# Performance work log

Hardware: AMD Instinct MI355X
Metric: run time of the kernel (lower is better)

The kernel has to match this reference:

```python
import jax, jax.numpy as jnp
import numpy as np
import math

POOLED_H = 2
POOLED_W = 64  # fixed: rois constructed so maxratio = POOLED_W / POOLED_H
NH = 256
NCLASS = 12  # len('0123456789.') + 1
C_IN = 512


def make_lstm_params(key, n_in, n_hidden):
    # torch nn.LSTM bidirectional: per direction W_ih [4H, in], W_hh [4H, H], b_ih, b_hh
    ks = jax.random.split(key, 8)
    s_i = 1.0 / np.sqrt(n_hidden)
    def u(k, shape):
        return jax.random.uniform(k, shape, jnp.float32, -s_i, s_i)
    p = {}
    for d, off in (('fw', 0), ('bw', 4)):
        p[d] = {
            'W_ih': u(ks[off + 0], (4 * n_hidden, n_in)),
            'W_hh': u(ks[off + 1], (4 * n_hidden, n_hidden)),
            'b_ih': u(ks[off + 2], (4 * n_hidden,)),
            'b_hh': u(ks[off + 3], (4 * n_hidden,)),
        }
    return p


def lstm_scan(x, p, n_hidden, reverse=False):
    # x: [T, B, n_in] -> [T, B, n_hidden]
    T, B, _ = x.shape
    W_ih, W_hh = p['W_ih'], p['W_hh']
    b = p['b_ih'] + p['b_hh']
    xg = jnp.einsum('tbi,gi->tbg', x, W_ih) + b  # [T,B,4H]

    def step(carry, xg_t):
        h, c = carry
        gates = xg_t + h @ W_hh.T
        i, f, g, o = jnp.split(gates, 4, axis=-1)
        i = jax.nn.sigmoid(i); f = jax.nn.sigmoid(f)
        g = jnp.tanh(g); o = jax.nn.sigmoid(o)
        c = f * c + i * g
        h = o * jnp.tanh(c)
        return (h, c), h

    h0 = jnp.zeros((B, n_hidden), x.dtype)
    c0 = jnp.zeros((B, n_hidden), x.dtype)
    _, hs = jax.lax.scan(step, (h0, c0), xg, reverse=reverse)
    return hs


def bilstm(x, p, n_hidden, W_emb, b_emb):
    hf = lstm_scan(x, p['fw'], n_hidden, reverse=False)
    hb = lstm_scan(x, p['bw'], n_hidden, reverse=True)
    h = jnp.concatenate([hf, hb], axis=-1)  # [T,B,2H]
    return h @ W_emb.T + b_emb


def roi_pool(base_feat, rois, pooled_h, pooled_w):
    # rois: [N,5] = [batch_idx, x1, y1, x2, y2] in feature coords (already scaled)
    # torch RoIPool: max pool over adaptive bins (spatial_scale=1).
    B, C, H, W = base_feat.shape

    def pool_one(roi):
        bi = roi[0].astype(jnp.int32)
        x1 = jnp.round(roi[1]).astype(jnp.int32)
        y1 = jnp.round(roi[2]).astype(jnp.int32)
        x2 = jnp.round(roi[3]).astype(jnp.int32)
        y2 = jnp.round(roi[4]).astype(jnp.int32)
        rw = jnp.maximum(x2 - x1 + 1, 1).astype(jnp.float32)
        rh = jnp.maximum(y2 - y1 + 1, 1).astype(jnp.float32)
        bin_h = rh / pooled_h
        bin_w = rw / pooled_w
        feat = base_feat[bi]  # [C,H,W]

        ph = jnp.arange(pooled_h)
        pw = jnp.arange(pooled_w)
        hstart = jnp.clip(jnp.floor(ph * bin_h).astype(jnp.int32) + y1, 0, H)
        hend = jnp.clip(jnp.ceil((ph + 1) * bin_h).astype(jnp.int32) + y1, 0, H)
        wstart = jnp.clip(jnp.floor(pw * bin_w).astype(jnp.int32) + x1, 0, W)
        wend = jnp.clip(jnp.ceil((pw + 1) * bin_w).astype(jnp.int32) + x1, 0, W)

        hh = jnp.arange(H)[None, :]
        ww = jnp.arange(W)[None, :]
        hmask = (hh >= hstart[:, None]) & (hh < hend[:, None])  # [ph,H]
        wmask = (ww >= wstart[:, None]) & (ww < wend[:, None])  # [pw,W]
        mask = hmask[:, None, :, None] & wmask[None, :, None, :]  # [ph,pw,H,W]
        neg = jnp.float32(-1e30)
        masked = jnp.where(mask[None], feat[:, None, None, :, :], neg)  # [C,ph,pw,H,W]
        pooled = masked.max(axis=(-2, -1))
        empty = ~mask.any(axis=(-2, -1))  # [ph,pw]
        return jnp.where(empty[None], 0.0, pooled)  # [C,ph,pw]

    return jax.vmap(pool_one)(rois)  # [N,C,ph,pw]


def setup_inputs() -> dict:
    key = jax.random.key(0)
    ks = jax.random.split(key, 10)
    B, C, H, W = 8, C_IN, 40, 160
    N = 32
    base_feat = jax.random.normal(ks[0], (B, C, H, W), jnp.float32)

    # rois normalized [bidx, x1, y1, x2, y2]; build so max aspect ratio = 32 -> pooled_w=64
    bidx = jax.random.randint(ks[1], (N,), 0, B).astype(jnp.float32)
    x1 = jax.random.uniform(ks[2], (N,), jnp.float32, 0.0, 0.3)
    y1 = jax.random.uniform(ks[3], (N,), jnp.float32, 0.0, 0.5)
    hgt = jax.random.uniform(ks[4], (N,), jnp.float32, 0.1, 0.3)
    # width/height ratio in normalized coords; after scaling by (W=160,H=40) feature
    # dims, ratio in feat coords = (w_n*160)/(h_n*40) = 4*w_n/h_n. Force max = 32.
    ratio = jax.random.uniform(ks[5], (N,), jnp.float32, 4.0, 32.0)
    ratio = ratio.at[0].set(32.0)
    wid_feat = ratio * (hgt * H)  # width in feature pixels
    wid = jnp.minimum(wid_feat / W, 0.99 - x1)
    # recompute so ratio exactly 32 at max: clamp keeps maxratio <= 32; pin roi 0
    wid = wid.at[0].set(jnp.minimum(32.0 * hgt[0] * H / W, 0.99 - x1[0]))
    hgt = hgt.at[0].set(wid[0] * W / (32.0 * H))
    x2 = x1 + wid
    y2 = jnp.minimum(y1 + hgt, 0.99)
    rois = jnp.stack([bidx, x1, y1, x2, y2], axis=1)

    text_length = jax.random.randint(ks[6], (1, N), 1, 8)
    text = jax.random.randint(ks[7], (1, 256), 1, NCLASS)  # labels 1..11

    # params
    p1 = make_lstm_params(ks[8], 1024, NH)
    p2 = make_lstm_params(ks[9], NH, NH)
    ke = jax.random.split(jax.random.key(1), 4)
    s1 = 1.0 / np.sqrt(2 * NH)
    W_emb1 = jax.random.uniform(ke[0], (NH, 2 * NH), jnp.float32, -s1, s1)
    b_emb1 = jax.random.uniform(ke[1], (NH,), jnp.float32, -s1, s1)
    W_emb2 = jax.random.uniform(ke[2], (NCLASS, 2 * NH), jnp.float32, -s1, s1)
    b_emb2 = jax.random.uniform(ke[3], (NCLASS,), jnp.float32, -s1, s1)

    params = {}
    for li, p in ((1, p1), (2, p2)):
        for d in ('fw', 'bw'):
            for n in ('W_ih', 'W_hh', 'b_ih', 'b_hh'):
                params[f'l{li}_{d}_{n}'] = p[d][n]
    params['W_emb1'] = W_emb1; params['b_emb1'] = b_emb1
    params['W_emb2'] = W_emb2; params['b_emb2'] = b_emb2

    return dict(base_feat=base_feat, text=text, text_length=text_length, rois=rois, **params)


def ctc_loss_sum(log_probs, labels, label_lengths):
    # log_probs: [T, B, K] log-softmax; labels: [B, Lmax] padded; blank = 0
    # standard CTC forward algorithm; returns sum of -log p over batch
    T, B, K = log_probs.shape
    Lmax = labels.shape[1]
    S = 2 * Lmax + 1
    # extended label sequence: blank, l1, blank, l2, ..., blank
    ext = jnp.zeros((B, S), jnp.int32)
    ext = ext.at[:, 1::2].set(labels.astype(jnp.int32))
    pos = jnp.arange(S)
    valid = pos[None, :] < (2 * label_lengths[:, None] + 1)

    # transition allowances
    same_as_2back = jnp.concatenate(
        [jnp.zeros((B, 2), bool), ext[:, 2:] == ext[:, :-2]], axis=1)
    is_blank = (ext == 0)
    allow_skip = (~is_blank) & (~same_as_2back)

    neg_inf = jnp.float32(-1e30)
    emit = jnp.take_along_axis(
        log_probs.transpose(1, 0, 2), ext[:, None, :].repeat(T, 1), axis=2
    ).transpose(1, 0, 2)  # [T, B, S]

    alpha0 = jnp.full((B, S), neg_inf)
    alpha0 = alpha0.at[:, 0].set(emit[0, :, 0])
    alpha0 = alpha0.at[:, 1].set(jnp.where(label_lengths > 0, emit[0, :, 1], neg_inf))

    def step(alpha, emit_t):
        a_prev1 = jnp.concatenate([jnp.full((B, 1), neg_inf), alpha[:, :-1]], axis=1)
        a_prev2 = jnp.concatenate([jnp.full((B, 2), neg_inf), alpha[:, :-2]], axis=1)
        a_prev2 = jnp.where(allow_skip, a_prev2, neg_inf)
        m = jnp.maximum(alpha, jnp.maximum(a_prev1, a_prev2))
        s = (jnp.exp(alpha - m) + jnp.exp(a_prev1 - m) + jnp.exp(a_prev2 - m))
        new = m + jnp.log(s) + emit_t
        new = jnp.where(valid, new, neg_inf)
        return new, None

    alpha_T, _ = jax.lax.scan(step, alpha0, emit[1:])
    end1 = 2 * label_lengths  # last blank
    end2 = 2 * label_lengths - 1  # last label
    aT1 = jnp.take_along_axis(alpha_T, end1[:, None], axis=1)[:, 0]
    aT2 = jnp.take_along_axis(alpha_T, jnp.maximum(end2, 0)[:, None], axis=1)[:, 0]
    aT2 = jnp.where(label_lengths > 0, aT2, neg_inf)
    m = jnp.maximum(aT1, aT2)
    logp = m + jnp.log(jnp.exp(aT1 - m) + jnp.exp(aT2 - m))
    return -jnp.sum(logp)


def reference(base_feat, text, text_length, rois,
              l1_fw_W_ih, l1_fw_W_hh, l1_fw_b_ih, l1_fw_b_hh,
              l1_bw_W_ih, l1_bw_W_hh, l1_bw_b_ih, l1_bw_b_hh,
              l2_fw_W_ih, l2_fw_W_hh, l2_fw_b_ih, l2_fw_b_hh,
              l2_bw_W_ih, l2_bw_W_hh, l2_bw_b_ih, l2_bw_b_hh,
              W_emb1, b_emb1, W_emb2, b_emb2):
    B, C, H, W = base_feat.shape
    rois = rois.at[:, jnp.array([1, 3])].multiply(W)
    rois = rois.at[:, jnp.array([2, 4])].multiply(H)
    pooled = roi_pool(base_feat, rois, POOLED_H, POOLED_W)  # [N,C,2,pw]
    N = pooled.shape[0]
    rnn_in = pooled.reshape(N, C * POOLED_H, POOLED_W).transpose(2, 0, 1)  # [T,N,1024]

    p1 = {'fw': dict(W_ih=l1_fw_W_ih, W_hh=l1_fw_W_hh, b_ih=l1_fw_b_ih, b_hh=l1_fw_b_hh),
          'bw': dict(W_ih=l1_bw_W_ih, W_hh=l1_bw_W_hh, b_ih=l1_bw_b_ih, b_hh=l1_bw_b_hh)}
    p2 = {'fw': dict(W_ih=l2_fw_W_ih, W_hh=l2_fw_W_hh, b_ih=l2_fw_b_ih, b_hh=l2_fw_b_hh),
          'bw': dict(W_ih=l2_bw_W_ih, W_hh=l2_bw_W_hh, b_ih=l2_bw_b_ih, b_hh=l2_bw_b_hh)}
    h1 = bilstm(rnn_in, p1, NH, W_emb1, b_emb1)
    preds = bilstm(h1, p2, NH, W_emb2, b_emb2)  # [T,N,nclass]

    log_probs = jax.nn.log_softmax(preds, axis=-1)
    tl = text_length[0].astype(jnp.int32)  # [N]
    # unflatten labels: text[0] holds concatenated labels; build padded [N, Lmax]
    Lmax = 8
    offsets = jnp.concatenate([jnp.zeros((1,), jnp.int32), jnp.cumsum(tl)[:-1]])
    idx = offsets[:, None] + jnp.arange(Lmax)[None, :]
    idx = jnp.clip(idx, 0, text.shape[1] - 1)
    labels = jnp.where(jnp.arange(Lmax)[None, :] < tl[:, None],
                       text[0][idx].astype(jnp.int32), 0)
    loss = ctc_loss_sum(log_probs, labels, tl) / N
    return loss
```

## Files before the change

### kernel.cpp

```cpp
#include <hip/hip_runtime.h>
#include <math.h>

#define TSTEPS 64
#define NSEQ   32
#define FH     40
#define FW     160

#define OFF_XGB    0u
#define OFF_RNNB   2097152u
#define OFF_W12B   3145728u
#define OFF_W22B   4194304u
#define OFF_WE1B   4456448u
#define OFF_WE2B   4521984u
#define OFF_PB1    4525056u
#define OFF_PB2    4527104u
#define OFF_W8L1F  4529152u
#define OFF_W8L1B  4594688u
#define OFF_W8L2F  4660224u
#define OFF_W8L2B  4725760u
#define OFF_HCB1   4791296u
#define OFF_HCB2   5315584u
#define OFF_H1B    5839872u
#define OFF_PREDS  6102016u

typedef __attribute__((ext_vector_type(8))) short short8;
typedef __attribute__((ext_vector_type(4))) float f32x4;
typedef __attribute__((ext_vector_type(4))) unsigned short ushort4v;
typedef __attribute__((ext_vector_type(4))) unsigned uint4v;

static __device__ inline unsigned short bf16c(float x) {
  union { float f; unsigned u; } v; v.f = x;
  unsigned r = v.u + 0x7fff + ((v.u >> 16) & 1);
  return (unsigned short)(r >> 16);
}
static __device__ inline float b2f(unsigned short u) {
  union { unsigned u; float f; } v; v.u = ((unsigned)u) << 16;
  return v.f;
}
static __device__ inline unsigned pk_bf16(float lo, float hi) {
  unsigned r;
  asm("v_cvt_pk_bf16_f32 %0, %1, %2" : "=v"(r) : "v"(lo), "v"(hi));
  return r;
}
static __device__ inline unsigned char fp8c(float x) {
  union { float f; unsigned u; } v; v.f = x;
  unsigned s = (v.u >> 24) & 0x80;
  float ax = fabsf(x);
  if (ax < 0.015625f) return (unsigned char)s;
  if (ax >= 448.0f) return (unsigned char)(s | 0x7e);
  unsigned e = (v.u >> 23) & 0xff;
  unsigned m = v.u & 0x7fffff;
  unsigned r = m + 0x7ffff + ((m >> 20) & 1);
  if (r >> 23) { e += 1; r = 0; }
  unsigned m3 = (r >> 20) & 7;
  int ee = (int)e - 127 + 7;
  if (ee > 15) return (unsigned char)(s | 0x7e);
  return (unsigned char)(s | (ee << 3) | m3);
}
static __device__ inline unsigned pk4_fp8(float a, float b, float c, float d) {
#if __has_builtin(__builtin_amdgcn_cvt_pk_fp8_f32)
  int r = __builtin_amdgcn_cvt_pk_fp8_f32(a, b, 0, false);
  r = __builtin_amdgcn_cvt_pk_fp8_f32(c, d, r, true);
  return (unsigned)r;
#else
  return (unsigned)fp8c(a) | ((unsigned)fp8c(b) << 8)
       | ((unsigned)fp8c(c) << 16) | ((unsigned)fp8c(d) << 24);
#endif
}

__global__ __launch_bounds__(256) void prep_kernel(
    const float* __restrict__ w1f, const float* __restrict__ w1b,
    const float* __restrict__ w2f, const float* __restrict__ w2b,
    const float* __restrict__ we1, const float* __restrict__ we2,
    const float* __restrict__ wh1f, const float* __restrict__ wh1b,
    const float* __restrict__ wh2f, const float* __restrict__ wh2b,
    const float* __restrict__ b1fi, const float* __restrict__ b1fh,
    const float* __restrict__ b1bi, const float* __restrict__ b1bh,
    const float* __restrict__ b2fi, const float* __restrict__ b2fh,
    const float* __restrict__ b2bi, const float* __restrict__ b2bh,
    unsigned short* __restrict__ w12b, unsigned short* __restrict__ w22b,
    unsigned short* __restrict__ we1o, unsigned short* __restrict__ we2o,
    unsigned char* __restrict__ o8l1f, unsigned char* __restrict__ o8l1b,
    unsigned char* __restrict__ o8l2f, unsigned char* __restrict__ o8l2b,
    float* __restrict__ pb1, float* __restrict__ pb2) {
  int b = blockIdx.x, tid = threadIdx.x;
  if (b < 2048) {
    const float* src = (b < 1024) ? w1f : w1b;
    unsigned short* dst = w12b + (size_t)((b < 1024) ? 0 : 1048576);
    int i = (b & 1023) * 256 + tid;
    int row = i >> 8, c4 = i & 255;
    int orow = (row & 255) * 4 + (row >> 8);
    float4 v = ((const float4*)src)[i];
    ushort4v o; o[0]=bf16c(v.x); o[1]=bf16c(v.y); o[2]=bf16c(v.z); o[3]=bf16c(v.w);
    *(ushort4v*)(dst + (size_t)orow * 1024 + c4 * 4) = o;
  } else if (b < 2560) {
    int bb = b - 2048;
    const float* src = (bb < 256) ? w2f : w2b;
    unsigned short* dst = w22b + (size_t)((bb < 256) ? 0 : 262144);
    int i = (bb & 255) * 256 + tid;
    int row = i >> 6, c4 = i & 63;
    int orow = (row & 255) * 4 + (row >> 8);
    float4 v = ((const float4*)src)[i];
    ushort4v o; o[0]=bf16c(v.x); o[1]=bf16c(v.y); o[2]=bf16c(v.z); o[3]=bf16c(v.w);
    *(ushort4v*)(dst + (size_t)orow * 256 + c4 * 4) = o;
  } else if (b < 2688) {
    int i = (b - 2560) * 256 + tid;
    int j = i >> 7, c4 = (i & 127) * 4;
    ushort4v o;
#pragma unroll
    for (int q = 0; q < 4; ++q) {
      int c = c4 + q;
      int d = c >> 8, k = c & 255;
      int u = (k >> 6) + (k & 63) * 4;
      o[q] = bf16c(we1[(size_t)j * 512 + d * 256 + u]);
    }
    ((ushort4v*)we1o)[i] = o;
  } else if (b < 2694) {
    int i = (b - 2688) * 256 + tid;
    int j = i >> 7, c4 = (i & 127) * 4;
    ushort4v o;
#pragma unroll
    for (int q = 0; q < 4; ++q) {
      int c = c4 + q;
      int d = c >> 8, k = c & 255;
      int u = (k >> 6) + (k & 63) * 4;
      o[q] = bf16c(we2[(size_t)j * 512 + d * 256 + u]);
    }
    ((ushort4v*)we2o)[i] = o;
  } else if (b < 3718) {
    int bb = b - 2694;
    int which = bb >> 8;
    const float* src = (which == 0) ? wh1f : (which == 1) ? wh1b
                     : (which == 2) ? wh2f : wh2b;
    unsigned char* dst = (which == 0) ? o8l1f : (which == 1) ? o8l1b
                       : (which == 2) ? o8l2f : o8l2b;
    int idx = (bb & 255) * 256 + tid;
    int row = idx >> 6, k4 = (idx & 63) * 4;
    const float* r = src + (size_t)row * 256;
    unsigned o = 0;
#pragma unroll
    for (int j = 0; j < 4; ++j) {
      int kp = k4 + j;
      int u = (kp >> 6) + (kp & 63) * 4;
      o |= ((unsigned)fp8c(r[u] * 64.0f)) << (8 * j);
    }
    ((unsigned*)dst)[idx] = o;
  } else if (b < 3726) {
    int m = (b - 3718) * 256 + tid;
    int dirq = m >> 10, mloc = m & 1023;
    int r = (mloc & 3) * 256 + (mloc >> 2);
    pb1[m] = dirq ? (b1bi[r] + b1bh[r]) : (b1fi[r] + b1fh[r]);
  } else {
    int m = (b - 3726) * 256 + tid;
    int dirq = m >> 10, mloc = m & 1023;
    int r = (mloc & 3) * 256 + (mloc >> 2);
    pb2[m] = dirq ? (b2bi[r] + b2bh[r]) : (b2fi[r] + b2fh[r]);
  }
}

__global__ __launch_bounds__(256) void roi_pool_kernel(
    const float* __restrict__ feat, const float* __restrict__ rois,
    unsigned short* __restrict__ rnn) {
  int n  = blockIdx.x;
  int cg = blockIdx.y;
  int tid = threadIdx.x;
  int pw = tid & 63, ph = (tid >> 6) & 1, cl = tid >> 7;
  int c = cg * 2 + cl;

  const float* r = rois + n * 5;
  int bi = (int)r[0];
  int x1 = (int)rintf(r[1] * (float)FW);
  int y1 = (int)rintf(r[2] * (float)FH);
  int x2 = (int)rintf(r[3] * (float)FW);
  int y2 = (int)rintf(r[4] * (float)FH);
  float rw = fmaxf((float)(x2 - x1 + 1), 1.0f);
  float rh = fmaxf((float)(y2 - y1 + 1), 1.0f);
  float bin_h = rh * 0.5f;
  float bin_w = rw * (1.0f / 64.0f);

  int hs = min(max((int)floorf((float)ph * bin_h) + y1, 0), FH);
  int he = min(max((int)ceilf((float)(ph + 1) * bin_h) + y1, 0), FH);
  int wst = min(max((int)floorf((float)pw * bin_w) + x1, 0), FW);
  int wen = min(max((int)ceilf((float)(pw + 1) * bin_w) + x1, 0), FW);

  float m = -1e30f;
  bool nonempty = (hs < he) && (wst < wen);
  const float* f = feat + ((size_t)bi * 512 + c) * (FH * FW);
  for (int h = hs; h < he; ++h) {
    const float* fr = f + h * FW;
    for (int w = wst; w < wen; ++w) m = fmaxf(m, fr[w]);
  }
  float out = nonempty ? m : 0.0f;
  rnn[((size_t)pw * NSEQ + n) * 1024 + c * 2 + ph] = bf16c(out);
}

#define GPITCH 40
__global__ __launch_bounds__(256) void gemm_bf16(
    const unsigned short* __restrict__ A, const unsigned short* __restrict__ B,
    float* __restrict__ Cf, unsigned short* __restrict__ Cb,
    int M, int N, int K,
    const float* __restrict__ bm1, const float* __restrict__ bn, int mode) {
  __shared__ unsigned short Al[128 * GPITCH];
  __shared__ unsigned short Bl[128 * GPITCH];
  int m0 = blockIdx.y * 128, n0 = blockIdx.x * 128;
  int tid = threadIdx.x;
  int wid = tid >> 6, l = tid & 63, ln15 = l & 15, kg = l >> 4;
  int wm = wid >> 1, wn = wid & 1;

  f32x4 acc[4][4];
#pragma unroll
  for (int i = 0; i < 4; ++i)
#pragma unroll
    for (int j = 0; j < 4; ++j)
#pragma unroll
      for (int q = 0; q < 4; ++q) acc[i][j][q] = 0.0f;

  for (int k0 = 0; k0 < K; k0 += 32) {
#pragma unroll
    for (int it = 0; it < 2; ++it) {
      int chunk = tid + it * 256;
      int row = chunk >> 2, part = chunk & 3;
      short8 va = *(const short8*)(A + (size_t)(m0 + row) * K + k0 + part * 8);
      *(short8*)(Al + row * GPITCH + part * 8) = va;
      short8 vb;
      if (n0 + row < N) {
        vb = *(const short8*)(B + (size_t)(n0 + row) * K + k0 + part * 8);
      } else {
#pragma unroll
        for (int q = 0; q < 8; ++q) vb[q] = 0;
      }
      *(short8*)(Bl + row * GPITCH + part * 8) = vb;
    }
    __syncthreads();

    short8 a[4], b[4];
#pragma unroll
    for (int mt = 0; mt < 4; ++mt)
      a[mt] = *(const short8*)(Al + (wm * 64 + mt * 16 + ln15) * GPITCH + kg * 8);
#pragma unroll
    for (int nt = 0; nt < 4; ++nt)
      b[nt] = *(const short8*)(Bl + (wn * 64 + nt * 16 + ln15) * GPITCH + kg * 8);
#pragma unroll
    for (int mt = 0; mt < 4; ++mt)
#pragma unroll
      for (int nt = 0; nt < 4; ++nt)
        acc[mt][nt] = __builtin_amdgcn_mfma_f32_16x16x32_bf16(a[mt], b[nt], acc[mt][nt], 0, 0, 0);
    __syncthreads();
  }

  if (mode == 5) {
#pragma unroll
    for (int mt = 0; mt < 4; ++mt) {
      int mbase = m0 + wm * 64 + mt * 16 + kg * 4;
      f32x4 pbv = *(const f32x4*)(bm1 + mbase);
      int dirq = mbase >> 10;
      int unit = (mbase & 1023) >> 2;
#pragma unroll
      for (int nt = 0; nt < 4; ++nt) {
        int col = n0 + wn * 64 + nt * 16 + ln15;
        int t = col >> 5, n = col & 31;
        ushort4v q;
#pragma unroll
        for (int j = 0; j < 4; ++j)
          q[j] = bf16c((acc[mt][nt][j] + pbv[j]) * 1024.0f);
        *(ushort4v*)(Cb + (size_t)dirq * 2097152u + ((t << 8) + unit) * 128 + n * 4) = q;
      }
    }
    return;
  }

#pragma unroll
  for (int mt = 0; mt < 4; ++mt) {
#pragma unroll
    for (int j = 0; j < 4; ++j) {
      int m = m0 + wm * 64 + mt * 16 + kg * 4 + j;
      float bmv = bm1 ? bm1[m] : 0.0f;
#pragma unroll
      for (int nt = 0; nt < 4; ++nt) {
        int n = n0 + wn * 64 + nt * 16 + ln15;
        if (n < N) {
          float v = acc[mt][nt][j] + bmv;
          if (bn) v += bn[n];
          if (mode == 1) Cb[(size_t)m * N + n] = bf16c(v);
          else Cf[(size_t)m * N + n] = v;
        }
      }
    }
  }
}

__global__ __launch_bounds__(512, 2) void lstm_layer8(
    const unsigned short* __restrict__ xgb,
    const unsigned char* __restrict__ w8fw,
    const unsigned char* __restrict__ w8bw,
    unsigned short* __restrict__ hcatb) {
  const int dir = blockIdx.x >> 1;
  const int nbase = (blockIdx.x & 1) * 16;
  const int tid = threadIdx.x;
  const int w = tid >> 6;
  const int l = tid & 63;
  const int ln15 = l & 15;
  const int kg = l >> 4;
  const int u_wave = w * 32;

  __shared__ unsigned char h8[2][16][256];

  const unsigned char* W8 = dir ? w8bw : w8fw;

  unsigned long long afrag[8][8];
  {
    int gate = ln15 & 3, du = ln15 >> 2;
#pragma unroll
    for (int mt = 0; mt < 8; ++mt) {
      const unsigned char* wr = W8 + (size_t)((gate << 8) + u_wave + mt * 4 + du) * 256;
#pragma unroll
      for (int kc = 0; kc < 8; ++kc)
        afrag[mt][kc] = *(const unsigned long long*)(wr + kc * 32 + kg * 8);
    }
  }

  const unsigned short* xgd = xgb + (size_t)dir * 2097152u;
  const int lane_off = (nbase + ln15) * 4;
  float cst[8] = {0.f, 0.f, 0.f, 0.f, 0.f, 0.f, 0.f, 0.f};
  f32x4 acc[8];
  ushort4v xnext[8];

  {
    int t0 = dir ? 63 : 0;
    const unsigned short* xb = xgd + (size_t)t0 * 32768 + lane_off;
#pragma unroll
    for (int mt = 0; mt < 8; ++mt)
      xnext[mt] = *(const ushort4v*)(xb + (u_wave + mt * 4 + kg) * 128);
#pragma unroll
    for (int mt = 0; mt < 8; ++mt)
#pragma unroll
      for (int j = 0; j < 4; ++j) acc[mt][j] = b2f(xnext[mt][j]);
  }

  const int swzw = (ln15 & 7) << 4;
  const int myslot = kg * 64 + w * 8;
  const float kNI = -1.0f / 1024.0f;
  const float kP2 = 2.0f / 1024.0f;

  for (int s = 0; s < TSTEPS; ++s) {
    const int t = dir ? (63 - s) : s;
    const int p = s & 1;

    if (s < TSTEPS - 1) {
      int tn2 = dir ? (t - 1) : (t + 1);
      const unsigned short* xb = xgd + (size_t)tn2 * 32768 + lane_off;
#pragma unroll
      for (int mt = 0; mt < 8; ++mt)
        xnext[mt] = *(const ushort4v*)(xb + (u_wave + mt * 4 + kg) * 128);
    }

    if (s > 0) {
      const unsigned char* hrow = &h8[p][ln15][0];
#pragma unroll
      for (int kc = 0; kc < 8; ++kc) {
        unsigned long long hb =
            *(const unsigned long long*)(hrow + ((kc * 32 + kg * 8) ^ swzw));
#pragma unroll
        for (int mt = 0; mt < 8; ++mt)
          acc[mt] = __builtin_amdgcn_mfma_f32_16x16x32_fp8_fp8(
              (long)afrag[mt][kc], (long)hb, acc[mt], 0, 0, 0);
      }
    }

    {
      float hv[8];
#pragma unroll
      for (int mt = 0; mt < 8; ++mt) {
        float gi = __builtin_amdgcn_rcpf(1.0f + __expf(acc[mt][0] * kNI));
        float gf = __builtin_amdgcn_rcpf(1.0f + __expf(acc[mt][1] * kNI));
        float gg = 1.0f - 2.0f * __builtin_amdgcn_rcpf(1.0f + __expf(acc[mt][2] * kP2));
        float go = __builtin_amdgcn_rcpf(1.0f + __expf(acc[mt][3] * kNI));
        float c = gf * cst[mt] + gi * gg;
        cst[mt] = c;
        hv[mt] = go * (1.0f - 2.0f * __builtin_amdgcn_rcpf(1.0f + __expf(2.0f * c)));
      }
      unsigned d0 = pk4_fp8(hv[0] * 16.f, hv[1] * 16.f, hv[2] * 16.f, hv[3] * 16.f);
      unsigned d1 = pk4_fp8(hv[4] * 16.f, hv[5] * 16.f, hv[6] * 16.f, hv[7] * 16.f);
      unsigned long long pk = (unsigned long long)d0 | ((unsigned long long)d1 << 32);
      *(unsigned long long*)(&h8[p ^ 1][ln15][0] + (myslot ^ swzw)) = pk;

      uint4v hb16;
      hb16[0] = pk_bf16(hv[0], hv[1]);
      hb16[1] = pk_bf16(hv[2], hv[3]);
      hb16[2] = pk_bf16(hv[4], hv[5]);
      hb16[3] = pk_bf16(hv[6], hv[7]);
      *(uint4v*)(hcatb + ((size_t)t * NSEQ + nbase + ln15) * 512 + dir * 256 + myslot) = hb16;

      if (s < TSTEPS - 1) {
#pragma unroll
        for (int mt = 0; mt < 8; ++mt)
#pragma unroll
          for (int j = 0; j < 4; ++j) acc[mt][j] = b2f(xnext[mt][j]);
      }
    }

    __syncthreads();
  }
}

#define CTC_S 17
__global__ __launch_bounds__(576) void ctc_kernel(
    const float* __restrict__ preds,
    const int* __restrict__ text,
    const int* __restrict__ text_len,
    float* __restrict__ out) {
  __shared__ float lp[TSTEPS][NSEQ][12];
  __shared__ float alpha[2][NSEQ][CTC_S];
  __shared__ int ext[NSEQ][CTC_S];
  __shared__ unsigned char allow[NSEQ][CTC_S];
  __shared__ unsigned char validm[NSEQ][CTC_S];
  __shared__ int tlsh[NSEQ];
  __shared__ float logp_sh[NSEQ];

  int tid = threadIdx.x;

  for (int r = tid; r < TSTEPS * NSEQ; r += 576) {
    const float* p = preds + (size_t)r * 12;
    float mx = p[0];
#pragma unroll
    for (int k = 1; k < 12; ++k) mx = fmaxf(mx, p[k]);
    float ssum = 0.f;
#pragma unroll
    for (int k = 0; k < 12; ++k) ssum += __expf(p[k] - mx);
    float ls = mx + __logf(ssum);
    int t = r >> 5, b = r & 31;
#pragma unroll
    for (int k = 0; k < 12; ++k) lp[t][b][k] = p[k] - ls;
  }
  if (tid < NSEQ) tlsh[tid] = text_len[tid];
  __syncthreads();

  int b = tid & 31, sIdx = tid >> 5;
  bool active = sIdx < CTC_S;

  if (active) {
    int tl = tlsh[b];
    int off = 0;
    for (int i = 0; i < b; ++i) off += tlsh[i];
    int e = 0;
    if (sIdx & 1) {
      int lbl = (sIdx - 1) >> 1;
      int idx = off + lbl;
      if (idx > 255) idx = 255;
      e = (lbl < tl) ? text[idx] : 0;
    }
    ext[b][sIdx] = e;
    validm[b][sIdx] = (sIdx < 2 * tl + 1) ? 1 : 0;
  }
  __syncthreads();
  if (active) {
    int e = ext[b][sIdx];
    bool same2 = (sIdx >= 2) && (e == ext[b][sIdx - 2]);
    allow[b][sIdx] = ((sIdx >= 2) && (e != 0) && !same2) ? 1 : 0;
    float a = -1e30f;
    if (sIdx == 0) a = lp[0][b][0];
    else if (sIdx == 1 && tlsh[b] > 0) a = lp[0][b][ext[b][1]];
    alpha[0][b][sIdx] = a;
  }
  __syncthreads();

  for (int t = 1; t < TSTEPS; ++t) {
    int cur = (t - 1) & 1, nxt = t & 1;
    if (active) {
      float a = alpha[cur][b][sIdx];
      float a1 = (sIdx >= 1) ? alpha[cur][b][sIdx - 1] : -1e30f;
      float a2 = (sIdx >= 2 && allow[b][sIdx]) ? alpha[cur][b][sIdx - 2] : -1e30f;
      float m = fmaxf(a, fmaxf(a1, a2));
      float ssum = __expf(a - m) + __expf(a1 - m) + __expf(a2 - m);
      float nv = m + __logf(ssum) + lp[t][b][ext[b][sIdx]];
      alpha[nxt][b][sIdx] = validm[b][sIdx] ? nv : -1e30f;
    }
    __syncthreads();
  }

  if (tid < NSEQ) {
    int tl = tlsh[b];
    float a1 = alpha[1][b][2 * tl];
    float a2 = (tl > 0) ? alpha[1][b][2 * tl - 1] : -1e30f;
    float m = fmaxf(a1, a2);
    logp_sh[b] = m + __logf(__expf(a1 - m) + __expf(a2 - m));
  }
  __syncthreads();
  if (tid == 0) {
    float ssum = 0.f;
    for (int i = 0; i < NSEQ; ++i) ssum += logp_sh[i];
    out[0] = -ssum / (float)NSEQ;
  }
}

extern "C" void kernel_launch(void* const* d_in, const int* in_sizes, int n_in,
                              void* d_out, int out_size, void* d_ws, size_t ws_size,
                              hipStream_t stream) {
  (void)in_sizes; (void)n_in; (void)out_size; (void)ws_size;
  const float* base_feat = (const float*)d_in[0];
  const int* text = (const int*)d_in[1];
  const int* text_len = (const int*)d_in[2];
  const float* rois = (const float*)d_in[3];
  const float* l1_fw_W_ih = (const float*)d_in[4];
  const float* l1_fw_W_hh = (const float*)d_in[5];
  const float* l1_fw_b_ih = (const float*)d_in[6];
  const float* l1_fw_b_hh = (const float*)d_in[7];
  const float* l1_bw_W_ih = (const float*)d_in[8];
  const float* l1_bw_W_hh = (const float*)d_in[9];
  const float* l1_bw_b_ih = (const float*)d_in[10];
  const float* l1_bw_b_hh = (const float*)d_in[11];
  const float* l2_fw_W_ih = (const float*)d_in[12];
  const float* l2_fw_W_hh = (const float*)d_in[13];
  const float* l2_fw_b_ih = (const float*)d_in[14];
  const float* l2_fw_b_hh = (const float*)d_in[15];
  const float* l2_bw_W_ih = (const float*)d_in[16];
  const float* l2_bw_W_hh = (const float*)d_in[17];
  const float* l2_bw_b_ih = (const float*)d_in[18];
  const float* l2_bw_b_hh = (const float*)d_in[19];
  const float* W_emb1 = (const float*)d_in[20];
  const float* b_emb1 = (const float*)d_in[21];
  const float* W_emb2 = (const float*)d_in[22];
  const float* b_emb2 = (const float*)d_in[23];

  float* ws = (float*)d_ws;
  unsigned short* xgb  = (unsigned short*)(ws + OFF_XGB);
  unsigned short* rnnb = (unsigned short*)(ws + OFF_RNNB);
  unsigned short* w12b = (unsigned short*)(ws + OFF_W12B);
  unsigned short* w22b = (unsigned short*)(ws + OFF_W22B);
  unsigned short* we1b = (unsigned short*)(ws + OFF_WE1B);
  unsigned short* we2b = (unsigned short*)(ws + OFF_WE2B);
  float* pb1 = ws + OFF_PB1;
  float* pb2 = ws + OFF_PB2;
  unsigned char* w8l1f = (unsigned char*)(ws + OFF_W8L1F);
  unsigned char* w8l1b = (unsigned char*)(ws + OFF_W8L1B);
  unsigned char* w8l2f = (unsigned char*)(ws + OFF_W8L2F);
  unsigned char* w8l2b = (unsigned char*)(ws + OFF_W8L2B);
  unsigned short* hcb1 = (unsigned short*)(ws + OFF_HCB1);
  unsigned short* hcb2 = (unsigned short*)(ws + OFF_HCB2);
  unsigned short* h1b  = (unsigned short*)(ws + OFF_H1B);
  float* preds = ws + OFF_PREDS;

  prep_kernel<<<3734, 256, 0, stream>>>(
      l1_fw_W_ih, l1_bw_W_ih, l2_fw_W_ih, l2_bw_W_ih, W_emb1, W_emb2,
      l1_fw_W_hh, l1_bw_W_hh, l2_fw_W_hh, l2_bw_W_hh,
      l1_fw_b_ih, l1_fw_b_hh, l1_bw_b_ih, l1_bw_b_hh,
      l2_fw_b_ih, l2_fw_b_hh, l2_bw_b_ih, l2_bw_b_hh,
      w12b, w22b, we1b, we2b, w8l1f, w8l1b, w8l2f, w8l2b, pb1, pb2);

  roi_pool_kernel<<<dim3(32, 256), 256, 0, stream>>>(base_feat, rois, rnnb);

  gemm_bf16<<<dim3(16, 16), 256, 0, stream>>>(w12b, rnnb, nullptr, xgb,
      2048, 2048, 1024, pb1, nullptr, 5);

  lstm_layer8<<<4, 512, 0, stream>>>(xgb, w8l1f, w8l1b, hcb1);

  gemm_bf16<<<dim3(2, 16), 256, 0, stream>>>(hcb1, we1b, nullptr, h1b,
      2048, 256, 512, nullptr, b_emb1, 1);

  gemm_bf16<<<dim3(16, 16), 256, 0, stream>>>(w22b, h1b, nullptr, xgb,
      2048, 2048, 256, pb2, nullptr, 5);

  lstm_layer8<<<4, 512, 0, stream>>>(xgb, w8l2f, w8l2b, hcb2);

  gemm_bf16<<<dim3(1, 16), 256, 0, stream>>>(hcb2, we2b, preds, nullptr,
      2048, 12, 512, nullptr, b_emb2, 0);

  ctc_kernel<<<1, 576, 0, stream>>>(preds, text, text_len, (float*)d_out);
}
```

Before: 459.0 us.

## Split LSTM recurrence across 16 waves and defer hidden-state global stores

The recurrent LSTM kernel now runs 1024 threads per block (16 waves), each handling 16 hidden units instead of 32. This halves the per-wave MFMA chain and gate math on the serial critical path. The bf16 hidden-state write to global memory is deferred to the start of the next step so it overlaps the MFMAs, and the exponentials use exp2 with folded log2e constants. The cost is more waves contending at the per-step barrier and a 4-byte LDS store per lane instead of 8 bytes.

```diff
diff --git a/kernel.cpp b/kernel.cpp
--- a/kernel.cpp
+++ b/kernel.cpp
@@ -26,7 +26,7 @@
 typedef __attribute__((ext_vector_type(8))) short short8;
 typedef __attribute__((ext_vector_type(4))) float f32x4;
 typedef __attribute__((ext_vector_type(4))) unsigned short ushort4v;
-typedef __attribute__((ext_vector_type(4))) unsigned uint4v;
+typedef __attribute__((ext_vector_type(2))) unsigned uint2v;
 
 static __device__ inline unsigned short bf16c(float x) {
   union { float f; unsigned u; } v; v.f = x;
@@ -289,7 +289,7 @@
   }
 }
 
-__global__ __launch_bounds__(512, 2) void lstm_layer8(
+__global__ __launch_bounds__(1024, 4) void lstm_layer9(
     const unsigned short* __restrict__ xgb,
     const unsigned char* __restrict__ w8fw,
     const unsigned char* __restrict__ w8bw,
@@ -301,17 +301,17 @@
   const int l = tid & 63;
   const int ln15 = l & 15;
   const int kg = l >> 4;
-  const int u_wave = w * 32;
+  const int u_wave = w * 16;
 
   __shared__ unsigned char h8[2][16][256];
 
   const unsigned char* W8 = dir ? w8bw : w8fw;
 
-  unsigned long long afrag[8][8];
+  unsigned long long afrag[4][8];
   {
     int gate = ln15 & 3, du = ln15 >> 2;
 #pragma unroll
-    for (int mt = 0; mt < 8; ++mt) {
+    for (int mt = 0; mt < 4; ++mt) {
       const unsigned char* wr = W8 + (size_t)((gate << 8) + u_wave + mt * 4 + du) * 256;
 #pragma unroll
       for (int kc = 0; kc < 8; ++kc)
@@ -321,36 +321,43 @@
 
   const unsigned short* xgd = xgb + (size_t)dir * 2097152u;
   const int lane_off = (nbase + ln15) * 4;
-  float cst[8] = {0.f, 0.f, 0.f, 0.f, 0.f, 0.f, 0.f, 0.f};
-  f32x4 acc[8];
-  ushort4v xnext[8];
+  float cst[4] = {0.f, 0.f, 0.f, 0.f};
+  f32x4 acc[4];
+  ushort4v xnext[4];
+  uint2v hpend;
+  int tpend = 0;
 
   {
     int t0 = dir ? 63 : 0;
     const unsigned short* xb = xgd + (size_t)t0 * 32768 + lane_off;
 #pragma unroll
-    for (int mt = 0; mt < 8; ++mt)
+    for (int mt = 0; mt < 4; ++mt)
       xnext[mt] = *(const ushort4v*)(xb + (u_wave + mt * 4 + kg) * 128);
 #pragma unroll
-    for (int mt = 0; mt < 8; ++mt)
+    for (int mt = 0; mt < 4; ++mt)
 #pragma unroll
       for (int j = 0; j < 4; ++j) acc[mt][j] = b2f(xnext[mt][j]);
   }
 
   const int swzw = (ln15 & 7) << 4;
-  const int myslot = kg * 64 + w * 8;
-  const float kNI = -1.0f / 1024.0f;
-  const float kP2 = 2.0f / 1024.0f;
+  const int myslot = kg * 64 + w * 4;
+  unsigned short* hc_lane = hcatb + (size_t)(nbase + ln15) * 512 + dir * 256 + myslot;
+  const float kNI = -1.442695041f / 1024.0f;
+  const float kP2 = 2.885390082f / 1024.0f;
+  const float k2L = 2.885390082f;
 
   for (int s = 0; s < TSTEPS; ++s) {
     const int t = dir ? (63 - s) : s;
     const int p = s & 1;
 
+    if (s > 0)
+      *(uint2v*)(hc_lane + (size_t)tpend * 16384) = hpend;
+
     if (s < TSTEPS - 1) {
       int tn2 = dir ? (t - 1) : (t + 1);
       const unsigned short* xb = xgd + (size_t)tn2 * 32768 + lane_off;
 #pragma unroll
-      for (int mt = 0; mt < 8; ++mt)
+      for (int mt = 0; mt < 4; ++mt)
         xnext[mt] = *(const ushort4v*)(xb + (u_wave + mt * 4 + kg) * 128);
     }
 
@@ -361,39 +368,34 @@
         unsigned long long hb =
             *(const unsigned long long*)(hrow + ((kc * 32 + kg * 8) ^ swzw));
 #pragma unroll
-        for (int mt = 0; mt < 8; ++mt)
+        for (int mt = 0; mt < 4; ++mt)
           acc[mt] = __builtin_amdgcn_mfma_f32_16x16x32_fp8_fp8(
               (long)afrag[mt][kc], (long)hb, acc[mt], 0, 0, 0);
       }
     }
 
     {
-      float hv[8];
-#pragma unroll
-      for (int mt = 0; mt < 8; ++mt) {
-        float gi = __builtin_amdgcn_rcpf(1.0f + __expf(acc[mt][0] * kNI));
-        float gf = __builtin_amdgcn_rcpf(1.0f + __expf(acc[mt][1] * kNI));
-        float gg = 1.0f - 2.0f * __builtin_amdgcn_rcpf(1.0f + __expf(acc[mt][2] * kP2));
-        float go = __builtin_amdgcn_rcpf(1.0f + __expf(acc[mt][3] * kNI));
+      float hv[4];
+#pragma unroll
+      for (int mt = 0; mt < 4; ++mt) {
+        float gi = __builtin_amdgcn_rcpf(1.0f + __builtin_exp2f(acc[mt][0] * kNI));
+        float gf = __builtin_amdgcn_rcpf(1.0f + __builtin_exp2f(acc[mt][1] * kNI));
+        float gg = 1.0f - 2.0f * __builtin_amdgcn_rcpf(1.0f + __builtin_exp2f(acc[mt][2] * kP2));
+        float go = __builtin_amdgcn_rcpf(1.0f + __builtin_exp2f(acc[mt][3] * kNI));
         float c = gf * cst[mt] + gi * gg;
         cst[mt] = c;
-        hv[mt] = go * (1.0f - 2.0f * __builtin_amdgcn_rcpf(1.0f + __expf(2.0f * c)));
+        hv[mt] = go * (1.0f - 2.0f * __builtin_amdgcn_rcpf(1.0f + __builtin_exp2f(c * k2L)));
       }
       unsigned d0 = pk4_fp8(hv[0] * 16.f, hv[1] * 16.f, hv[2] * 16.f, hv[3] * 16.f);
-      unsigned d1 = pk4_fp8(hv[4] * 16.f, hv[5] * 16.f, hv[6] * 16.f, hv[7] * 16.f);
-      unsigned long long pk = (unsigned long long)d0 | ((unsigned long long)d1 << 32);
-      *(unsigned long long*)(&h8[p ^ 1][ln15][0] + (myslot ^ swzw)) = pk;
-
-      uint4v hb16;
-      hb16[0] = pk_bf16(hv[0], hv[1]);
-      hb16[1] = pk_bf16(hv[2], hv[3]);
-      hb16[2] = pk_bf16(hv[4], hv[5]);
-      hb16[3] = pk_bf16(hv[6], hv[7]);
-      *(uint4v*)(hcatb + ((size_t)t * NSEQ + nbase + ln15) * 512 + dir * 256 + myslot) = hb16;
+      *(unsigned*)(&h8[p ^ 1][ln15][0] + (myslot ^ swzw)) = d0;
+
+      hpend[0] = pk_bf16(hv[0], hv[1]);
+      hpend[1] = pk_bf16(hv[2], hv[3]);
+      tpend = t;
 
       if (s < TSTEPS - 1) {
 #pragma unroll
-        for (int mt = 0; mt < 8; ++mt)
+        for (int mt = 0; mt < 4; ++mt)
 #pragma unroll
           for (int j = 0; j < 4; ++j) acc[mt][j] = b2f(xnext[mt][j]);
       }
@@ -401,6 +403,8 @@
 
     __syncthreads();
   }
+
+  *(uint2v*)(hc_lane + (size_t)tpend * 16384) = hpend;
 }
 
 #define CTC_S 17
@@ -552,7 +556,7 @@
   gemm_bf16<<<dim3(16, 16), 256, 0, stream>>>(w12b, rnnb, nullptr, xgb,
       2048, 2048, 1024, pb1, nullptr, 5);
 
-  lstm_layer8<<<4, 512, 0, stream>>>(xgb, w8l1f, w8l1b, hcb1);
+  lstm_layer9<<<4, 1024, 0, stream>>>(xgb, w8l1f, w8l1b, hcb1);
 
   gemm_bf16<<<dim3(2, 16), 256, 0, stream>>>(hcb1, we1b, nullptr, h1b,
       2048, 256, 512, nullptr, b_emb1, 1);
@@ -560,7 +564,7 @@
   gemm_bf16<<<dim3(16, 16), 256, 0, stream>>>(w22b, h1b, nullptr, xgb,
       2048, 2048, 256, pb2, nullptr, 5);
 
-  lstm_layer8<<<4, 512, 0, stream>>>(xgb, w8l2f, w8l2b, hcb2);
+  lstm_layer9<<<4, 1024, 0, stream>>>(xgb, w8l2f, w8l2b, hcb2);
 
   gemm_bf16<<<dim3(1, 16), 256, 0, stream>>>(hcb2, we2b, preds, nullptr,
       2048, 12, 512, nullptr, b_emb2, 0);
```

New measurement: 481.2 us. 1.05x slower.
